# Optimization experiments

Measured on AMD Instinct MI355X. Metric: run time of the kernel, lower is better.

The kernel has to match this reference:

```python
import jax, jax.numpy as jnp
import numpy as np

B, N, C = 8, 4096, 512
NH = 8
HD = C // NH
EPS = 1e-12  # torch F.normalize default eps


def setup_inputs() -> dict:
    key = jax.random.key(0)
    ks = jax.random.split(key, 6)
    x = jax.random.normal(ks[0], (B, N, C), dtype=jnp.float32)
    x_out = jax.random.normal(ks[1], (B, N, C), dtype=jnp.float32)
    # params: torch Linear weight [out,in]; store as [in,out] for x @ W
    W_qkv = jax.random.normal(ks[2], (C, 3 * C), dtype=jnp.float32) * (1.0 / np.sqrt(C))
    temperature = jnp.ones((NH, 1, 1), dtype=jnp.float32)
    W_proj = jax.random.normal(ks[3], (C, C), dtype=jnp.float32) * (1.0 / np.sqrt(C))
    b_proj = jax.random.normal(ks[4], (C,), dtype=jnp.float32) * 0.01
    return {"x": x, "x_out": x_out, "W_qkv": W_qkv, "temperature": temperature,
            "W_proj": W_proj, "b_proj": b_proj, "H": 64, "W": 64}


def _l2norm(t):
    # F.normalize(t, dim=-1): t / max(||t||_2, eps)
    n = jnp.sqrt(jnp.sum(t * t, axis=-1, keepdims=True))
    return t / jnp.maximum(n, EPS)


def reference(x, x_out, W_qkv, temperature, W_proj, b_proj, H, W):
    b, n, c = x.shape
    nh = temperature.shape[0]
    hd = c // nh
    qkv = (x @ W_qkv).reshape(b, n, 3, nh, hd).transpose(2, 0, 3, 1, 4)  # [3,B,nh,N,hd]
    q, k, v = qkv[0], qkv[1], qkv[2]
    # transpose to channel-attention layout [B,nh,hd,N]
    q = jnp.swapaxes(q, -2, -1)
    k = jnp.swapaxes(k, -2, -1)
    v = jnp.swapaxes(v, -2, -1)
    q = _l2norm(q)
    k = _l2norm(k)
    # cross-covariance attention over channels: [B,nh,hd,hd]
    attn = jnp.einsum('bhcn,bhdn->bhcd', q, k) * temperature
    attn = jax.nn.softmax(attn, axis=-1)
    out = jnp.einsum('bhcd,bhdn->bhcn', attn, v)  # [B,nh,hd,N]
    out = out.transpose(0, 3, 1, 2).reshape(b, n, c)
    return out @ W_proj + b_proj
```

## Files before the change

### kernel.cpp

```cpp
#include <hip/hip_runtime.h>
#include <hip/hip_bf16.h>

typedef __attribute__((ext_vector_type(8))) short short8;
typedef __attribute__((ext_vector_type(4))) float f32x4;

#define BQ 8
#define SEQ 4096
#define CH 512
#define NHD 8
#define HD 64
#define K3C 1536
#define MTOK 32768
#define NSPL 8

__device__ __forceinline__ float bfu2f(unsigned int u) {
  u <<= 16;
  float f;
  __builtin_memcpy(&f, &u, 4);
  return f;
}
__device__ __forceinline__ unsigned short f2bfu(float x) {
  __hip_bfloat16 h = __float2bfloat16(x);
  unsigned short u;
  __builtin_memcpy(&u, &h, 2);
  return u;
}

__device__ __forceinline__ void gload_lds16(const void* g, void* l) {
  __builtin_amdgcn_global_load_lds(
      (const __attribute__((address_space(1))) unsigned int*)g,
      (__attribute__((address_space(3))) unsigned int*)l, 16, 0, 0);
}

__global__ __launch_bounds__(256) void cast_f32_bf16(const float* __restrict__ in,
                                                     unsigned short* __restrict__ out, int n4) {
  int stride = gridDim.x * blockDim.x;
  for (int i = blockIdx.x * blockDim.x + threadIdx.x; i < n4; i += stride) {
    float4 v = reinterpret_cast<const float4*>(in)[i];
    ushort4 o;
    o.x = f2bfu(v.x); o.y = f2bfu(v.y); o.z = f2bfu(v.z); o.w = f2bfu(v.w);
    reinterpret_cast<ushort4*>(out)[i] = o;
  }
}

__global__ __launch_bounds__(256) void transpose_cast(const float* __restrict__ in,
                                                      unsigned short* __restrict__ out,
                                                      int R, int Cc) {
  __shared__ float tile[32][33];
  const int tx = threadIdx.x, ty = threadIdx.y;
  const int c0 = blockIdx.x * 32, r0 = blockIdx.y * 32;
  #pragma unroll
  for (int dy = 0; dy < 32; dy += 8)
    tile[ty + dy][tx] = in[(size_t)(r0 + ty + dy) * Cc + (c0 + tx)];
  __syncthreads();
  #pragma unroll
  for (int dy = 0; dy < 32; dy += 8)
    out[(size_t)(c0 + ty + dy) * R + (r0 + tx)] = f2bfu(tile[tx][ty + dy]);
}

template <int MODE>
__global__ __launch_bounds__(512, 4) void gemm256(const unsigned short* __restrict__ A,
                                                  const unsigned short* __restrict__ Bt,
                                                  void* __restrict__ out0,
                                                  void* __restrict__ out1,
                                                  const float* __restrict__ bias,
                                                  int M, int Nn, int Kk, int nbx) {
  __shared__ __align__(16) char lds[73728];
  const int nwg = gridDim.x;
  int wg = blockIdx.x;
  wg = (wg & 7) * (nwg >> 3) + (wg >> 3);
  const int bx = wg % nbx, by = wg / nbx;
  const int m0 = by * 256, n0 = bx * 128;

  const int tid = threadIdx.x, wave = tid >> 6, lane = tid & 63;
  const int wr = wave >> 1, wc = wave & 1;
  const int l15 = lane & 15, lg = lane >> 4;
  const int T = Kk >> 5;

  f32x4 acc[4][4] = {};
  short8 af[4], bf[4];

  const int prowA = tid >> 3, sA = tid & 7;
  const int slinA = sA ^ (prowA & 7);
  const int mA = ((slinA >> 2) << 7) + prowA, kA = (slinA & 3) << 3;
  const int prow2 = prowA + 64;
  const int slin2 = sA ^ (prow2 & 7);
  const int m2 = ((slin2 >> 2) << 7) + prow2, k2 = (slin2 & 3) << 3;
  const int prowB = tid >> 3, sB = tid & 7;
  const int slinB = sB ^ (prowB & 7);
  const int nB = ((slinB >> 2) << 6) + prowB, kB = (slinB & 3) << 3;
  const int woff = wave * 1024;

  const int bidx = m0 >> 12;
  const unsigned short* Bt2 = Bt + (size_t)bidx * 262144;
  const int nrow1 = (m0 & 4095) + mA, nrow2 = (m0 & 4095) + m2;

  auto stageAB = [&](int kt, char* buf) {
    if (MODE == 2) {
      const unsigned short* Abase =
          A + (size_t)(bidx * 8 + (kt >> 6)) * 4096 * 64 + (kt & 32);
      gload_lds16(Abase + (size_t)nrow1 * 64 + kA, buf + woff);
      gload_lds16(Abase + (size_t)nrow2 * 64 + k2, buf + 8192 + woff);
      gload_lds16(Bt2 + (size_t)(n0 + nB) * Kk + kt + kB, buf + 16384 + woff);
    } else {
      gload_lds16(A + (size_t)(m0 + mA) * Kk + kt + kA, buf + woff);
      gload_lds16(A + (size_t)(m0 + m2) * Kk + kt + k2, buf + 8192 + woff);
      gload_lds16(Bt + (size_t)(n0 + nB) * Kk + kt + kB, buf + 16384 + woff);
    }
  };

  auto dsA = [&](const char* bufc) {
    #pragma unroll
    for (int fr = 0; fr < 4; ++fr) {
      const int m = wr * 64 + fr * 16 + l15;
      const int prow = m & 127;
      const int s = ((m >> 7) * 4 + lg) ^ (l15 & 7);
      af[fr] = *reinterpret_cast<const short8*>(bufc + prow * 128 + (s << 4));
    }
  };
  auto dsB = [&](const char* bufc) {
    #pragma unroll
    for (int fc = 0; fc < 4; ++fc) {
      const int prow = fc * 16 + l15;
      const int s = (wc * 4 + lg) ^ (l15 & 7);
      bf[fc] = *reinterpret_cast<const short8*>(bufc + 16384 + prow * 128 + (s << 4));
    }
  };

  stageAB(0, lds);
  stageAB(32, lds + 24576);
  asm volatile("s_waitcnt vmcnt(3)" ::: "memory");
  __builtin_amdgcn_s_barrier();

  char* p0 = lds;
  char* p1 = lds + 24576;
  char* p2 = lds + 49152;

  for (int t = 0; t < T; ++t) {
    dsA(p0);
    dsB(p0);
    const bool st2 = (t + 2 < T);
    if (st2) stageAB((t + 2) << 5, p2);
    __builtin_amdgcn_s_setprio(1);
    #pragma unroll
    for (int fr = 0; fr < 4; ++fr)
      #pragma unroll
      for (int fc = 0; fc < 4; ++fc)
        acc[fr][fc] = __builtin_amdgcn_mfma_f32_16x16x32_bf16(
            af[fr], bf[fc], acc[fr][fc], 0, 0, 0);
    __builtin_amdgcn_s_setprio(0);
    if (t + 1 < T) {
      if (st2) asm volatile("s_waitcnt vmcnt(3)" ::: "memory");
      else     asm volatile("s_waitcnt vmcnt(0)" ::: "memory");
      __builtin_amdgcn_s_barrier();
    }
    char* tmp = p0; p0 = p1; p1 = p2; p2 = tmp;
  }

  if (MODE == 2) {
    #pragma unroll
    for (int fr = 0; fr < 4; ++fr)
      #pragma unroll
      for (int fc = 0; fc < 4; ++fc) {
        const int row0 = m0 + wr * 64 + fr * 16 + lg * 4;
        const int col = n0 + wc * 64 + fc * 16 + l15;
        #pragma unroll
        for (int v = 0; v < 4; ++v)
          reinterpret_cast<float*>(out0)[(size_t)(row0 + v) * Nn + col] =
              acc[fr][fc][v] + bias[col];
      }
  } else if (n0 < 1024) {
    #pragma unroll
    for (int p = 0; p < 2; ++p) {
      __builtin_amdgcn_s_barrier();
      if (wc == p) {
        #pragma unroll
        for (int fr = 0; fr < 4; ++fr)
          #pragma unroll
          for (int fc = 0; fc < 4; ++fc) {
            const int tok = wr * 64 + fr * 16 + lg * 4;
            const int cl = fc * 16 + l15;
            ushort4 o;
            o.x = f2bfu(acc[fr][fc][0]);
            o.y = f2bfu(acc[fr][fc][1]);
            o.z = f2bfu(acc[fr][fc][2]);
            o.w = f2bfu(acc[fr][fc][3]);
            const int byte = cl * 512 + ((tok * 2) ^ ((cl & 7) << 4));
            *reinterpret_cast<ushort4*>(lds + byte) = o;
          }
      }
      __builtin_amdgcn_s_barrier();
      #pragma unroll
      for (int it = 0; it < 4; ++it) {
        const int cl = it * 16 + (tid >> 5);
        const int ns = (tid & 31) * 8;
        const int byte = cl * 512 + ((ns * 2) ^ ((cl & 7) << 4));
        short8 val = *reinterpret_cast<const short8*>(lds + byte);
        const int gcol = n0 + p * 64 + cl;
        const int sel = gcol >> 9, rem = gcol & 511;
        const int bh = (m0 >> 12) * 8 + (rem >> 6), cc = rem & 63;
        *reinterpret_cast<short8*>(&reinterpret_cast<unsigned short*>(out0)[
            ((size_t)sel * 4096 + bh * 64 + cc) * 4096 + (m0 & 4095) + ns]) = val;
      }
    }
  } else {
    #pragma unroll
    for (int fr = 0; fr < 4; ++fr)
      #pragma unroll
      for (int fc = 0; fc < 4; ++fc) {
        const int row0 = m0 + wr * 64 + fr * 16 + lg * 4;
        const int col = n0 + wc * 64 + fc * 16 + l15;
        const int rem = col & 511, hh = rem >> 6, cc = rem & 63;
        const int bb = row0 >> 12, nseq = row0 & 4095;
        const int bh = bb * 8 + hh;
        #pragma unroll
        for (int v = 0; v < 4; ++v)
          reinterpret_cast<unsigned short*>(out1)[
              ((size_t)bh * 4096 + nseq + v) * 64 + cc] =
              f2bfu(acc[fr][fc][v]);
      }
  }
}

__global__ __launch_bounds__(256) void attn_qk(const unsigned short* __restrict__ qkT,
                                               float* __restrict__ rawp,
                                               float* __restrict__ normp) {
  const int bh = blockIdx.x, s = blockIdx.y;
  const int tid = threadIdx.x, w = tid >> 6, lane = tid & 63;
  const int l15 = lane & 15, lg = lane >> 4;
  const int nbase = s * 512 + w * 128;
  const unsigned short* qrow = qkT + (size_t)(bh * 64) * 4096;
  const unsigned short* krow = qkT + (size_t)(4096 + bh * 64) * 4096;

  __shared__ float red[4][64][64];
  __shared__ float nrm[4][2][64];

  f32x4 acc[4][4] = {};
  float sq[4] = {0.f, 0.f, 0.f, 0.f}, sk[4] = {0.f, 0.f, 0.f, 0.f};

  #pragma unroll
  for (int kc = 0; kc < 2; ++kc) {
    short8 aq[4][2], bk[4][2];
    #pragma unroll
    for (int fr = 0; fr < 4; ++fr)
      #pragma unroll
      for (int ks = 0; ks < 2; ++ks) {
        const size_t off = (size_t)(fr * 16 + l15) * 4096 + nbase + (kc * 2 + ks) * 32 + lg * 8;
        aq[fr][ks] = *reinterpret_cast<const short8*>(&qrow[off]);
        bk[fr][ks] = *reinterpret_cast<const short8*>(&krow[off]);
      }
    #pragma unroll
    for (int ks = 0; ks < 2; ++ks)
      #pragma unroll
      for (int fr = 0; fr < 4; ++fr)
        #pragma unroll
        for (int fc = 0; fc < 4; ++fc)
          acc[fr][fc] = __builtin_amdgcn_mfma_f32_16x16x32_bf16(
              aq[fr][ks], bk[fc][ks], acc[fr][fc], 0, 0, 0);
    #pragma unroll
    for (int fr = 0; fr < 4; ++fr)
      #pragma unroll
      for (int ks = 0; ks < 2; ++ks)
        #pragma unroll
        for (int j = 0; j < 8; ++j) {
          const float fq = bfu2f((unsigned short)aq[fr][ks][j]);
          const float fk = bfu2f((unsigned short)bk[fr][ks][j]);
          sq[fr] = fmaf(fq, fq, sq[fr]);
          sk[fr] = fmaf(fk, fk, sk[fr]);
        }
  }

  #pragma unroll
  for (int fr = 0; fr < 4; ++fr) {
    sq[fr] += __shfl_xor(sq[fr], 16); sq[fr] += __shfl_xor(sq[fr], 32);
    sk[fr] += __shfl_xor(sk[fr], 16); sk[fr] += __shfl_xor(sk[fr], 32);
  }
  if (lane < 16) {
    #pragma unroll
    for (int fr = 0; fr < 4; ++fr) {
      nrm[w][0][fr * 16 + lane] = sq[fr];
      nrm[w][1][fr * 16 + lane] = sk[fr];
    }
  }
  #pragma unroll
  for (int fr = 0; fr < 4; ++fr)
    #pragma unroll
    for (int fc = 0; fc < 4; ++fc)
      #pragma unroll
      for (int v = 0; v < 4; ++v)
        red[w][fr * 16 + lg * 4 + v][fc * 16 + l15] = acc[fr][fc][v];
  __syncthreads();

  const float* rf = &red[0][0][0];
  float* rp = rawp + ((size_t)s * 64 + bh) * 4096;
  for (int i = tid; i < 4096; i += 256)
    rp[i] = rf[i] + rf[4096 + i] + rf[8192 + i] + rf[12288 + i];
  const float* nf = &nrm[0][0][0];
  if (tid < 128) {
    float* np = normp + ((size_t)s * 64 + bh) * 128;
    np[tid] = nf[tid] + nf[128 + tid] + nf[256 + tid] + nf[384 + tid];
  }
}

__global__ __launch_bounds__(64) void attn_finalize(const float* __restrict__ rawp,
                                                    const float* __restrict__ normp,
                                                    const float* __restrict__ temperature,
                                                    float* __restrict__ Pmat) {
  const int bh = blockIdx.x, c8 = blockIdx.y, h = bh & 7;
  const int d = threadIdx.x;
  float nq = 0.f, nk = 0.f;
  for (int s = 0; s < NSPL; ++s) {
    nq += normp[((size_t)s * 64 + bh) * 128 + d];
    nk += normp[((size_t)s * 64 + bh) * 128 + 64 + d];
  }
  nq = fmaxf(sqrtf(nq), 1e-12f);
  nk = fmaxf(sqrtf(nk), 1e-12f);
  const float t = temperature[h];
  for (int i = 0; i < 8; ++i) {
    const int c = c8 * 8 + i;
    float r = 0.f;
    for (int s = 0; s < NSPL; ++s)
      r += rawp[((size_t)s * 64 + bh) * 4096 + c * 64 + d];
    const float nqc = __shfl(nq, c);
    float v = r * t / (nqc * nk);
    float m = v;
    #pragma unroll
    for (int off = 32; off > 0; off >>= 1) m = fmaxf(m, __shfl_xor(m, off));
    float e = __expf(v - m);
    float ssum = e;
    #pragma unroll
    for (int off = 32; off > 0; off >>= 1) ssum += __shfl_xor(ssum, off);
    Pmat[(size_t)bh * 4096 + c * 64 + d] = e / ssum;
  }
}

__global__ __launch_bounds__(256) void wmod_kernel(const float* __restrict__ Pmat,
                                                   const float* __restrict__ Wproj,
                                                   unsigned short* __restrict__ WmodT) {
  const int bh = blockIdx.x, jt = blockIdx.y;
  const int b = bh >> 3, h = bh & 7;
  const int tid = threadIdx.x;
  __shared__ float PL[64][64];
  __shared__ float WT[64][65];
  for (int i = tid; i < 4096; i += 256) PL[i >> 6][i & 63] = Pmat[(size_t)bh * 4096 + i];
  for (int i = tid; i < 4096; i += 256) {
    const int c = i >> 6, j = i & 63;
    WT[c][j] = Wproj[(size_t)(h * 64 + c) * 512 + jt * 64 + j];
  }
  __syncthreads();
  const int d = tid & 63, jq = tid >> 6;
  #pragma unroll
  for (int jl = jq * 16; jl < jq * 16 + 16; ++jl) {
    float acc = 0.f;
    #pragma unroll
    for (int c = 0; c < 64; ++c) acc = fmaf(PL[c][d], WT[c][jl], acc);
    WmodT[((size_t)b * 512 + jt * 64 + jl) * 512 + h * 64 + d] = f2bfu(acc);
  }
}

extern "C" void kernel_launch(void* const* d_in, const int* in_sizes, int n_in,
                              void* d_out, int out_size, void* d_ws, size_t ws_size,
                              hipStream_t stream) {
  const float* x = (const float*)d_in[0];
  const float* Wqkv = (const float*)d_in[2];
  const float* temp = (const float*)d_in[3];
  const float* Wproj = (const float*)d_in[4];
  const float* bproj = (const float*)d_in[5];
  float* out = (float*)d_out;

  char* w = (char*)d_ws;
  unsigned short* xb = (unsigned short*)w;    w += (size_t)MTOK * CH * 2;
  unsigned short* wqT = (unsigned short*)w;   w += (size_t)K3C * CH * 2;
  unsigned short* qkT = (unsigned short*)w;   w += (size_t)2 * 64 * 64 * 4096 * 2;
  unsigned short* vb = (unsigned short*)w;    w += (size_t)64 * 4096 * 64 * 2;
  float* rawp = (float*)w;                    w += (size_t)NSPL * 64 * 4096 * 4;
  float* normp = (float*)w;                   w += (size_t)NSPL * 64 * 128 * 4;
  float* Pmat = (float*)w;                    w += (size_t)64 * 4096 * 4;
  unsigned short* WmodT = (unsigned short*)w; w += (size_t)BQ * CH * CH * 2;

  cast_f32_bf16<<<2048, 256, 0, stream>>>(x, xb, MTOK * CH / 4);
  transpose_cast<<<dim3(K3C / 32, CH / 32), dim3(32, 8), 0, stream>>>(Wqkv, wqT, CH, K3C);
  gemm256<0><<<1536, 512, 0, stream>>>(xb, wqT, qkT, vb, nullptr, MTOK, K3C, CH, 12);
  attn_qk<<<dim3(64, 8), 256, 0, stream>>>(qkT, rawp, normp);
  attn_finalize<<<dim3(64, 8), 64, 0, stream>>>(rawp, normp, temp, Pmat);
  wmod_kernel<<<dim3(64, 8), 256, 0, stream>>>(Pmat, Wproj, WmodT);
  gemm256<2><<<512, 512, 0, stream>>>(vb, WmodT, out, nullptr, bproj, MTOK, CH, CH, 4);
}
```

Baseline: 158.6 us.

## Stage QK tiles through swizzled double-buffered LDS and drop cross-wave reduction

Rewrites attn_qk so each block loads coalesced 128-column chunks of Q and K into XOR-swizzled, double-buffered shared memory. Each wave owns 16 Q rows against all 64 K rows, which removes the 64KB cross-wave reduction buffer and the extra sync. Partial sums and norms are written directly to global memory. attn_finalize is widened to 256 threads so four waves split the rows of each block. In exchange it adds two syncs per chunk, and the LDS use limits occupancy.

```diff
diff --git a/kernel.cpp b/kernel.cpp
--- a/kernel.cpp
+++ b/kernel.cpp
@@ -228,87 +228,98 @@
   const int bh = blockIdx.x, s = blockIdx.y;
   const int tid = threadIdx.x, w = tid >> 6, lane = tid & 63;
   const int l15 = lane & 15, lg = lane >> 4;
-  const int nbase = s * 512 + w * 128;
-  const unsigned short* qrow = qkT + (size_t)(bh * 64) * 4096;
-  const unsigned short* krow = qkT + (size_t)(4096 + bh * 64) * 4096;
-
-  __shared__ float red[4][64][64];
-  __shared__ float nrm[4][2][64];
-
-  f32x4 acc[4][4] = {};
-  float sq[4] = {0.f, 0.f, 0.f, 0.f}, sk[4] = {0.f, 0.f, 0.f, 0.f};
-
-  #pragma unroll
-  for (int kc = 0; kc < 2; ++kc) {
-    short8 aq[4][2], bk[4][2];
-    #pragma unroll
-    for (int fr = 0; fr < 4; ++fr)
-      #pragma unroll
-      for (int ks = 0; ks < 2; ++ks) {
-        const size_t off = (size_t)(fr * 16 + l15) * 4096 + nbase + (kc * 2 + ks) * 32 + lg * 8;
-        aq[fr][ks] = *reinterpret_cast<const short8*>(&qrow[off]);
-        bk[fr][ks] = *reinterpret_cast<const short8*>(&krow[off]);
-      }
-    #pragma unroll
-    for (int ks = 0; ks < 2; ++ks)
-      #pragma unroll
-      for (int fr = 0; fr < 4; ++fr)
-        #pragma unroll
-        for (int fc = 0; fc < 4; ++fc)
-          acc[fr][fc] = __builtin_amdgcn_mfma_f32_16x16x32_bf16(
-              aq[fr][ks], bk[fc][ks], acc[fr][fc], 0, 0, 0);
-    #pragma unroll
-    for (int fr = 0; fr < 4; ++fr)
-      #pragma unroll
-      for (int ks = 0; ks < 2; ++ks)
-        #pragma unroll
-        for (int j = 0; j < 8; ++j) {
-          const float fq = bfu2f((unsigned short)aq[fr][ks][j]);
-          const float fk = bfu2f((unsigned short)bk[fr][ks][j]);
-          sq[fr] = fmaf(fq, fq, sq[fr]);
-          sk[fr] = fmaf(fk, fk, sk[fr]);
-        }
-  }
-
-  #pragma unroll
-  for (int fr = 0; fr < 4; ++fr) {
-    sq[fr] += __shfl_xor(sq[fr], 16); sq[fr] += __shfl_xor(sq[fr], 32);
-    sk[fr] += __shfl_xor(sk[fr], 16); sk[fr] += __shfl_xor(sk[fr], 32);
-  }
+  const unsigned short* qrow = qkT + (size_t)(bh * 64) * 4096 + s * 512;
+  const unsigned short* krow = qkT + (size_t)(4096 + bh * 64) * 4096 + s * 512;
+
+  __shared__ __align__(16) char lds[65536];
+
+  const int srow = tid >> 4;
+  const int sslot = tid & 15;
+  uint4 qreg[4], kreg[4];
+
+  auto loadChunk = [&](int nb) {
+    #pragma unroll
+    for (int r4 = 0; r4 < 4; ++r4) {
+      const int r = srow + r4 * 16;
+      qreg[r4] = *reinterpret_cast<const uint4*>(&qrow[(size_t)r * 4096 + nb + sslot * 8]);
+      kreg[r4] = *reinterpret_cast<const uint4*>(&krow[(size_t)r * 4096 + nb + sslot * 8]);
+    }
+  };
+  auto writeChunk = [&](char* buf) {
+    #pragma unroll
+    for (int r4 = 0; r4 < 4; ++r4) {
+      const int r = srow + r4 * 16;
+      const int byte = r * 256 + ((sslot ^ (r & 7)) << 4);
+      *reinterpret_cast<uint4*>(buf + byte) = qreg[r4];
+      *reinterpret_cast<uint4*>(buf + 16384 + byte) = kreg[r4];
+    }
+  };
+
+  f32x4 acc[4] = {};
+  float sq = 0.f, sk = 0.f;
+
+  loadChunk(0);
+  writeChunk(lds);
+  __syncthreads();
+
+  for (int chunk = 0; chunk < 4; ++chunk) {
+    char* bufc = lds + (chunk & 1) * 32768;
+    if (chunk < 3) loadChunk((chunk + 1) * 128);
+    #pragma unroll
+    for (int ks = 0; ks < 4; ++ks) {
+      const int rA = w * 16 + l15;
+      const int slotq = ((ks << 2) + lg);
+      short8 af = *reinterpret_cast<const short8*>(
+          bufc + rA * 256 + ((slotq ^ (rA & 7)) << 4));
+      short8 bf[4];
+      #pragma unroll
+      for (int fc = 0; fc < 4; ++fc) {
+        const int rB = fc * 16 + l15;
+        bf[fc] = *reinterpret_cast<const short8*>(
+            bufc + 16384 + rB * 256 + ((slotq ^ (rB & 7)) << 4));
+      }
+      #pragma unroll
+      for (int fc = 0; fc < 4; ++fc)
+        acc[fc] = __builtin_amdgcn_mfma_f32_16x16x32_bf16(af, bf[fc], acc[fc], 0, 0, 0);
+      #pragma unroll
+      for (int j = 0; j < 8; ++j) {
+        const float fq = bfu2f((unsigned short)af[j]);
+        const float fk = bfu2f((unsigned short)bf[w][j]);
+        sq = fmaf(fq, fq, sq);
+        sk = fmaf(fk, fk, sk);
+      }
+    }
+    if (chunk < 3) {
+      __syncthreads();
+      writeChunk(lds + ((chunk + 1) & 1) * 32768);
+      __syncthreads();
+    }
+  }
+
+  sq += __shfl_xor(sq, 16); sq += __shfl_xor(sq, 32);
+  sk += __shfl_xor(sk, 16); sk += __shfl_xor(sk, 32);
+  float* np = normp + ((size_t)s * 64 + bh) * 128;
   if (lane < 16) {
-    #pragma unroll
-    for (int fr = 0; fr < 4; ++fr) {
-      nrm[w][0][fr * 16 + lane] = sq[fr];
-      nrm[w][1][fr * 16 + lane] = sk[fr];
-    }
-  }
-  #pragma unroll
-  for (int fr = 0; fr < 4; ++fr)
-    #pragma unroll
-    for (int fc = 0; fc < 4; ++fc)
-      #pragma unroll
-      for (int v = 0; v < 4; ++v)
-        red[w][fr * 16 + lg * 4 + v][fc * 16 + l15] = acc[fr][fc][v];
-  __syncthreads();
-
-  const float* rf = &red[0][0][0];
+    np[w * 16 + lane] = sq;
+    np[64 + w * 16 + lane] = sk;
+  }
+
   float* rp = rawp + ((size_t)s * 64 + bh) * 4096;
-  for (int i = tid; i < 4096; i += 256)
-    rp[i] = rf[i] + rf[4096 + i] + rf[8192 + i] + rf[12288 + i];
-  const float* nf = &nrm[0][0][0];
-  if (tid < 128) {
-    float* np = normp + ((size_t)s * 64 + bh) * 128;
-    np[tid] = nf[tid] + nf[128 + tid] + nf[256 + tid] + nf[384 + tid];
-  }
-}
-
-__global__ __launch_bounds__(64) void attn_finalize(const float* __restrict__ rawp,
-                                                    const float* __restrict__ normp,
-                                                    const float* __restrict__ temperature,
-                                                    float* __restrict__ Pmat) {
+  #pragma unroll
+  for (int fc = 0; fc < 4; ++fc)
+    #pragma unroll
+    for (int v = 0; v < 4; ++v)
+      rp[(w * 16 + lg * 4 + v) * 64 + fc * 16 + l15] = acc[fc][v];
+}
+
+__global__ __launch_bounds__(256) void attn_finalize(const float* __restrict__ rawp,
+                                                     const float* __restrict__ normp,
+                                                     const float* __restrict__ temperature,
+                                                     float* __restrict__ Pmat) {
   const int bh = blockIdx.x, c8 = blockIdx.y, h = bh & 7;
-  const int d = threadIdx.x;
+  const int tid = threadIdx.x, w = tid >> 6, d = tid & 63;
   float nq = 0.f, nk = 0.f;
+  #pragma unroll
   for (int s = 0; s < NSPL; ++s) {
     nq += normp[((size_t)s * 64 + bh) * 128 + d];
     nk += normp[((size_t)s * 64 + bh) * 128 + 64 + d];
@@ -316,13 +327,15 @@
   nq = fmaxf(sqrtf(nq), 1e-12f);
   nk = fmaxf(sqrtf(nk), 1e-12f);
   const float t = temperature[h];
-  for (int i = 0; i < 8; ++i) {
-    const int c = c8 * 8 + i;
-    float r = 0.f;
+  #pragma unroll
+  for (int i = 0; i < 2; ++i) {
+    const int c = c8 * 8 + w * 2 + i;
+    float rs = 0.f;
+    #pragma unroll
     for (int s = 0; s < NSPL; ++s)
-      r += rawp[((size_t)s * 64 + bh) * 4096 + c * 64 + d];
+      rs += rawp[((size_t)s * 64 + bh) * 4096 + c * 64 + d];
     const float nqc = __shfl(nq, c);
-    float v = r * t / (nqc * nk);
+    float v = rs * t / (nqc * nk);
     float m = v;
     #pragma unroll
     for (int off = 32; off > 0; off >>= 1) m = fmaxf(m, __shfl_xor(m, off));
@@ -382,7 +395,7 @@
   transpose_cast<<<dim3(K3C / 32, CH / 32), dim3(32, 8), 0, stream>>>(Wqkv, wqT, CH, K3C);
   gemm256<0><<<1536, 512, 0, stream>>>(xb, wqT, qkT, vb, nullptr, MTOK, K3C, CH, 12);
   attn_qk<<<dim3(64, 8), 256, 0, stream>>>(qkT, rawp, normp);
-  attn_finalize<<<dim3(64, 8), 64, 0, stream>>>(rawp, normp, temp, Pmat);
+  attn_finalize<<<dim3(64, 8), 256, 0, stream>>>(rawp, normp, temp, Pmat);
   wmod_kernel<<<dim3(64, 8), 256, 0, stream>>>(Pmat, Wproj, WmodT);
   gemm256<2><<<512, 512, 0, stream>>>(vb, WmodT, out, nullptr, bproj, MTOK, CH, CH, 4);
 }
```

Measured after the change: 347.4 us. +119.0%, slower.
